# Kernel tuning notes

Hardware: AMD Instinct MI355X
Metric: run time of the kernel (lower is better)

## Reference

```python
import jax, jax.numpy as jnp
import numpy as np


def setup_inputs() -> dict:
    key = jax.random.key(0)
    k1, k2, k3, k4 = jax.random.split(key, 4)
    n, d, h, w = 16, 512, 64, 64
    m, kcodes = 4, 256
    dm = d // m  # 128
    latent = jax.random.normal(k1, (n, d, h, w), dtype=jnp.float32)
    codebook = jax.random.normal(k2, (m, kcodes, dm), dtype=jnp.float32)
    wq = jax.random.normal(k3, (m, dm, dm), dtype=jnp.float32) / np.sqrt(dm)
    wk = jax.random.normal(k4, (m, dm, dm), dtype=jnp.float32) / np.sqrt(dm)
    return {"latent": latent, "codebook": codebook, "wq": wq, "wk": wk}


def reference(latent, codebook, wq, wk):
    # latent: [n, d, h, w]; codebook: [m, k, dm]; wq/wk: [m, dm, dm]
    n, d, h, w = latent.shape
    m, kcodes, dm = codebook.shape
    # NCHW -> NHWC -> [n, h, w, m, dm]
    q = jnp.transpose(latent, (0, 2, 3, 1)).reshape(n, h, w, m, dm)
    # per-group query projection: q @ wq^T (einsum 'nhwmd,mcd->nhwmc')
    q = jnp.einsum('nhwmd,mcd->nhwmc', q, wq)
    # per-group key projection of codebook: 'mkd,mcd->mkc'
    keys = jnp.einsum('mkd,mcd->mkc', codebook, wk)
    # dot-product scores over code dim, then argmax -> code indices
    scores = jnp.einsum('nhwmd,mkd->nhwmk', q, keys)
    code = jnp.argmax(scores, axis=-1).astype(jnp.uint8)
    return code
```

## Files before the change

### kernel.cpp

```cpp
#include <hip/hip_runtime.h>


#define MM   4
#define KC   256
#define DM   128
#define HW   4096
#define WW_  64
#define EPS  0.045f
#define WL_CAP 65536
#define RSH  136

typedef _Float16 f16x8 __attribute__((ext_vector_type(8)));
typedef _Float16 f16x4 __attribute__((ext_vector_type(4)));
typedef _Float16 f16x2 __attribute__((ext_vector_type(2)));
typedef float    f32x4 __attribute__((ext_vector_type(4)));
typedef float    f32x2 __attribute__((ext_vector_type(2)));

__global__ __launch_bounds__(128) void a_kernel(const float* __restrict__ wk,
                                                const float* __restrict__ wq,
                                                double* __restrict__ A) {
    int me = blockIdx.x;
    int d  = threadIdx.x;
    int m  = me >> 7;
    int e  = me & 127;
    const float* wkm = wk + (size_t)m * DM * DM + e;
    const float* wqm = wq + (size_t)m * DM * DM + d;
    double s0 = 0.0, s1 = 0.0, s2 = 0.0, s3 = 0.0;
#pragma unroll 8
    for (int c = 0; c < DM; c += 4) {
        s0 = fma((double)wkm[(size_t)(c+0) * DM], (double)wqm[(size_t)(c+0) * DM], s0);
        s1 = fma((double)wkm[(size_t)(c+1) * DM], (double)wqm[(size_t)(c+1) * DM], s1);
        s2 = fma((double)wkm[(size_t)(c+2) * DM], (double)wqm[(size_t)(c+2) * DM], s2);
        s3 = fma((double)wkm[(size_t)(c+3) * DM], (double)wqm[(size_t)(c+3) * DM], s3);
    }
    A[(size_t)me * DM + d] = (s0 + s1) + (s2 + s3);
}

__global__ __launch_bounds__(128) void keff_kernel(const float* __restrict__ cb,
                                                   const double* __restrict__ A,
                                                   double* __restrict__ keffdT,
                                                   _Float16* __restrict__ keff16) {
    int mk = blockIdx.x;
    int d  = threadIdx.x;
    int m  = mk >> 8;
    int k  = mk & 255;
    const float*  cbr = cb + (size_t)mk * DM;
    const double* Am  = A + (size_t)m * DM * DM + d;
    double s0 = 0.0, s1 = 0.0, s2 = 0.0, s3 = 0.0;
#pragma unroll 8
    for (int e = 0; e < DM; e += 4) {
        s0 = fma((double)cbr[e+0], Am[(size_t)(e+0) * DM], s0);
        s1 = fma((double)cbr[e+1], Am[(size_t)(e+1) * DM], s1);
        s2 = fma((double)cbr[e+2], Am[(size_t)(e+2) * DM], s2);
        s3 = fma((double)cbr[e+3], Am[(size_t)(e+3) * DM], s3);
    }
    double s = (s0 + s1) + (s2 + s3);
    keffdT[((size_t)m * DM + d) * KC + k] = s;
    keff16[(size_t)mk * DM + d] = (_Float16)s;
}

__global__ __launch_bounds__(512, 4) void argmax_mfma(const float* __restrict__ latent,
                                                      const _Float16* __restrict__ keff16,
                                                      int* __restrict__ out,
                                                      int* __restrict__ wl_cnt,
                                                      int* __restrict__ wl) {
    __shared__ _Float16 lq[2][64 * RSH];
    __shared__ float pbv[64][8];
    __shared__ float psv[64][8];
    __shared__ int   pbi[64][8];

    int blk  = blockIdx.x;
    int n    = blk >> 5;
    int m    = (blk >> 3) & 3;
    int hg   = blk & 7;
    int tid  = threadIdx.x;
    int wave = tid >> 6;
    int lane = tid & 63;
    int col  = lane & 15;
    int quad = lane >> 4;
    int w2   = (tid & 31) * 2;
    int db   = (tid >> 5) * 8;

    f16x8 Af[2][4];
    {
        const _Float16* kbase = keff16 + ((size_t)m * KC + wave * 32) * DM;
#pragma unroll
        for (int t = 0; t < 2; ++t)
#pragma unroll
            for (int s = 0; s < 4; ++s)
                Af[t][s] = *(const f16x8*)(kbase + (size_t)(t * 16 + col) * DM + s * 32 + quad * 8);
    }

    const float* lp0 = latent + ((size_t)(n * 512 + m * DM)) * HW + (size_t)(hg * 8) * WW_;

    {
        f32x2 pf[8];
#pragma unroll
        for (int pp = 0; pp < 8; ++pp)
            pf[pp] = *(const f32x2*)(lp0 + (size_t)(db + pp) * HW + w2);
#pragma unroll
        for (int j = 0; j < 2; ++j) {
            f16x8 v;
#pragma unroll
            for (int pp = 0; pp < 8; ++pp) v[pp] = (_Float16)pf[pp][j];
            *(f16x8*)&lq[0][(size_t)(w2 + j) * RSH + db] = v;
        }
    }
    __syncthreads();

    for (int r = 0; r < 8; ++r) {
        int cur = r & 1;

        f32x2 pf[8];
        if (r < 7) {
            const float* lp = lp0 + (size_t)(r + 1) * WW_;
#pragma unroll
            for (int pp = 0; pp < 8; ++pp)
                pf[pp] = *(const f32x2*)(lp + (size_t)(db + pp) * HW + w2);
        }

#pragma unroll
        for (int p = 0; p < 4; ++p) {
            f16x8 Bf[4];
#pragma unroll
            for (int s = 0; s < 4; ++s)
                Bf[s] = *(const f16x8*)&lq[cur][(size_t)(p * 16 + col) * RSH + s * 32 + quad * 8];
            f32x4 acc[2];
#pragma unroll
            for (int t = 0; t < 2; ++t) {
                f32x4 c = (f32x4){0.f, 0.f, 0.f, 0.f};
                c = __builtin_amdgcn_mfma_f32_16x16x32_f16(Af[t][0], Bf[0], c, 0, 0, 0);
                c = __builtin_amdgcn_mfma_f32_16x16x32_f16(Af[t][1], Bf[1], c, 0, 0, 0);
                c = __builtin_amdgcn_mfma_f32_16x16x32_f16(Af[t][2], Bf[2], c, 0, 0, 0);
                c = __builtin_amdgcn_mfma_f32_16x16x32_f16(Af[t][3], Bf[3], c, 0, 0, 0);
                acc[t] = c;
            }
            float bv = acc[0][0];
            int   bi = wave * 32 + quad * 4;
            float sv = -3.0e38f;
#pragma unroll
            for (int t = 0; t < 2; ++t)
#pragma unroll
                for (int g = 0; g < 4; ++g) {
                    if (t == 0 && g == 0) continue;
                    float v   = acc[t][g];
                    int   idx = wave * 32 + t * 16 + quad * 4 + g;
                    if (v > bv)      { sv = bv; bv = v; bi = idx; }
                    else if (v > sv) sv = v;
                }
#pragma unroll
            for (int off = 16; off < 64; off <<= 1) {
                float ov = __shfl_xor(bv, off);
                int   oi = __shfl_xor(bi, off);
                float os = __shfl_xor(sv, off);
                bool  take  = (ov > bv) || (ov == bv && oi < bi);
                float loser = take ? bv : ov;
                sv = fmaxf(fmaxf(sv, os), loser);
                if (take) { bv = ov; bi = oi; }
            }
            if (quad == 0) {
                int P = p * 16 + col;
                pbv[P][wave] = bv; psv[P][wave] = sv; pbi[P][wave] = bi;
            }
        }
        __syncthreads();

        if (tid < 64) {
            int   P  = tid;
            float bv = pbv[P][0]; float sv = psv[P][0]; int bi = pbi[P][0];
#pragma unroll
            for (int wv = 1; wv < 8; ++wv) {
                float ov = pbv[P][wv]; float os = psv[P][wv]; int oi = pbi[P][wv];
                bool  take  = (ov > bv) || (ov == bv && oi < bi);
                float loser = take ? bv : ov;
                sv = fmaxf(fmaxf(sv, os), loser);
                if (take) { bv = ov; bi = oi; }
            }
            int h   = hg * 8 + r;
            int pix = (((n * 64 + h) * 64) + P) * MM + m;
            out[pix] = bi;
            if (bv - sv < EPS) {
                int slot = atomicAdd(wl_cnt, 1);
                if (slot < WL_CAP) wl[slot] = pix;
            }
        }

        if (r < 7) {
#pragma unroll
            for (int j = 0; j < 2; ++j) {
                f16x8 v;
#pragma unroll
                for (int pp = 0; pp < 8; ++pp) v[pp] = (_Float16)pf[pp][j];
                *(f16x8*)&lq[cur ^ 1][(size_t)(w2 + j) * RSH + db] = v;
            }
        }
        __syncthreads();
    }
}

__global__ __launch_bounds__(256) void rescue_kernel(const float* __restrict__ latent,
                                                     const double* __restrict__ keffdT,
                                                     const int* __restrict__ wl_cnt,
                                                     const int* __restrict__ wl,
                                                     int* __restrict__ out) {
    __shared__ double sq[DM];
    __shared__ double svals[256];
    __shared__ int    sidx[256];
    int cnt = *wl_cnt;
    if (cnt > WL_CAP) cnt = WL_CAP;
    int t = threadIdx.x;
    for (int i = blockIdx.x; i < cnt; i += gridDim.x) {
        int pix = wl[i];
        int m   = pix & 3;
        int rem = pix >> 2;
        int w   = rem & 63;
        int bh  = rem >> 6;
        int n   = bh >> 6;
        int h   = bh & 63;
        const float* lp = latent + ((size_t)(n * 512 + m * DM)) * HW + h * WW_ + w;
        if (t < DM) sq[t] = (double)lp[(size_t)t * HW];
        __syncthreads();
        const double* kr = keffdT + (size_t)m * DM * KC + t;
        double s0 = 0.0, s1 = 0.0, s2 = 0.0, s3 = 0.0;
#pragma unroll 8
        for (int d = 0; d < DM; d += 4) {
            s0 = fma(sq[d+0], kr[(size_t)(d+0) * KC], s0);
            s1 = fma(sq[d+1], kr[(size_t)(d+1) * KC], s1);
            s2 = fma(sq[d+2], kr[(size_t)(d+2) * KC], s2);
            s3 = fma(sq[d+3], kr[(size_t)(d+3) * KC], s3);
        }
        svals[t] = (s0 + s1) + (s2 + s3);
        sidx[t]  = t;
        __syncthreads();
        for (int stp = 128; stp > 0; stp >>= 1) {
            if (t < stp) {
                double vo = svals[t + stp], vm = svals[t];
                int io = sidx[t + stp], im = sidx[t];
                if (vo > vm || (vo == vm && io < im)) { svals[t] = vo; sidx[t] = io; }
            }
            __syncthreads();
        }
        if (t == 0) out[pix] = sidx[0];
        __syncthreads();
    }
}

extern "C" void kernel_launch(void* const* d_in, const int* in_sizes, int n_in,
                              void* d_out, int out_size, void* d_ws, size_t ws_size,
                              hipStream_t stream) {
    const float* latent = (const float*)d_in[0];
    const float* cb     = (const float*)d_in[1];
    const float* wq     = (const float*)d_in[2];
    const float* wk     = (const float*)d_in[3];
    int* out = (int*)d_out;

    char* ws = (char*)d_ws;
    double*   A      = (double*)ws;     ws += (size_t)MM * DM * DM * sizeof(double);
    double*   keffdT = (double*)ws;     ws += (size_t)MM * DM * KC * sizeof(double);
    _Float16* keff16 = (_Float16*)ws;   ws += (size_t)MM * KC * DM * sizeof(_Float16);
    int*      wl_cnt = (int*)ws;        ws += 256;
    int*      wl     = (int*)ws;

    hipMemsetAsync(wl_cnt, 0, sizeof(int), stream);
    a_kernel<<<MM * DM, 128, 0, stream>>>(wk, wq, A);
    keff_kernel<<<MM * KC, 128, 0, stream>>>(cb, A, keffdT, keff16);
    argmax_mfma<<<512, 512, 0, stream>>>(latent, keff16, out, wl_cnt, wl);
    rescue_kernel<<<1024, 256, 0, stream>>>(latent, keffdT, wl_cnt, wl, out);
}
```

Before: 276.3 us.

## Parallelize per-row argmax merge, split worklist per group, batch rescue pixels

In the MFMA argmax kernel the cross-wave merge now uses all 512 threads with shuffles instead of 64 threads looping. The partial buffers are double-buffered so one __syncthreads per row can be dropped, and the next-row LDS store is moved before the barrier. The rescue worklist is split per group m with separate padded counters to reduce atomic contention. Each rescue block now handles 4 pixels at once, so every keff row load is shared across them. Capacity per group drops to 16384 entries, which could overflow if near-tie pixels cluster in one group.

Result: faster. 253.6 us (-8.2%).

```diff
diff --git a/kernel.cpp b/kernel.cpp
--- a/kernel.cpp
+++ b/kernel.cpp
@@ -7,7 +7,8 @@
 #define HW   4096
 #define WW_  64
 #define EPS  0.045f
-#define WL_CAP 65536
+#define WLC  16384
+#define RPB  4
 #define RSH  136
 
 typedef _Float16 f16x8 __attribute__((ext_vector_type(8)));
@@ -65,9 +66,9 @@
                                                       int* __restrict__ wl_cnt,
                                                       int* __restrict__ wl) {
     __shared__ _Float16 lq[2][64 * RSH];
-    __shared__ float pbv[64][8];
-    __shared__ float psv[64][8];
-    __shared__ int   pbi[64][8];
+    __shared__ float pbv[2][64][8];
+    __shared__ float psv[2][64][8];
+    __shared__ int   pbi[2][64][8];
 
     int blk  = blockIdx.x;
     int n    = blk >> 5;
@@ -160,41 +161,47 @@
             }
             if (quad == 0) {
                 int P = p * 16 + col;
-                pbv[P][wave] = bv; psv[P][wave] = sv; pbi[P][wave] = bi;
-            }
-        }
-        __syncthreads();
-
-        if (tid < 64) {
-            int   P  = tid;
-            float bv = pbv[P][0]; float sv = psv[P][0]; int bi = pbi[P][0];
-#pragma unroll
-            for (int wv = 1; wv < 8; ++wv) {
-                float ov = pbv[P][wv]; float os = psv[P][wv]; int oi = pbi[P][wv];
+                pbv[cur][P][wave] = bv; psv[cur][P][wave] = sv; pbi[cur][P][wave] = bi;
+            }
+        }
+
+        if (r < 7) {
+#pragma unroll
+            for (int j = 0; j < 2; ++j) {
+                f16x8 v;
+#pragma unroll
+                for (int pp = 0; pp < 8; ++pp) v[pp] = (_Float16)pf[pp][j];
+                *(f16x8*)&lq[cur ^ 1][(size_t)(w2 + j) * RSH + db] = v;
+            }
+        }
+        __syncthreads();
+
+        {
+            int P    = tid >> 3;
+            int slot = tid & 7;
+            float bv = pbv[cur][P][slot];
+            float sv = psv[cur][P][slot];
+            int   bi = pbi[cur][P][slot];
+#pragma unroll
+            for (int off = 1; off < 8; off <<= 1) {
+                float ov = __shfl_xor(bv, off);
+                int   oi = __shfl_xor(bi, off);
+                float os = __shfl_xor(sv, off);
                 bool  take  = (ov > bv) || (ov == bv && oi < bi);
                 float loser = take ? bv : ov;
                 sv = fmaxf(fmaxf(sv, os), loser);
                 if (take) { bv = ov; bi = oi; }
             }
-            int h   = hg * 8 + r;
-            int pix = (((n * 64 + h) * 64) + P) * MM + m;
-            out[pix] = bi;
-            if (bv - sv < EPS) {
-                int slot = atomicAdd(wl_cnt, 1);
-                if (slot < WL_CAP) wl[slot] = pix;
-            }
-        }
-
-        if (r < 7) {
-#pragma unroll
-            for (int j = 0; j < 2; ++j) {
-                f16x8 v;
-#pragma unroll
-                for (int pp = 0; pp < 8; ++pp) v[pp] = (_Float16)pf[pp][j];
-                *(f16x8*)&lq[cur ^ 1][(size_t)(w2 + j) * RSH + db] = v;
-            }
-        }
-        __syncthreads();
+            if (slot == 0) {
+                int h   = hg * 8 + r;
+                int pix = (((n * 64 + h) * 64) + P) * MM + m;
+                out[pix] = bi;
+                if (bv - sv < EPS) {
+                    int s_ = atomicAdd(wl_cnt + m * 16, 1);
+                    if (s_ < WLC) wl[m * WLC + s_] = pix;
+                }
+            }
+        }
     }
 }
 
@@ -203,44 +210,63 @@
                                                      const int* __restrict__ wl_cnt,
                                                      const int* __restrict__ wl,
                                                      int* __restrict__ out) {
-    __shared__ double sq[DM];
-    __shared__ double svals[256];
-    __shared__ int    sidx[256];
-    int cnt = *wl_cnt;
-    if (cnt > WL_CAP) cnt = WL_CAP;
-    int t = threadIdx.x;
-    for (int i = blockIdx.x; i < cnt; i += gridDim.x) {
-        int pix = wl[i];
-        int m   = pix & 3;
+    __shared__ double sq[RPB][DM];
+    __shared__ double sval[256][RPB];
+    __shared__ int    sidx[256][RPB];
+    __shared__ int    spix[RPB];
+    int b   = blockIdx.x;
+    int m   = b & 3;
+    int t   = threadIdx.x;
+    int cnt = wl_cnt[m * 16];
+    if (cnt > WLC) cnt = WLC;
+    const int*    wlm = wl + m * WLC;
+    const double* krm = keffdT + (size_t)m * DM * KC + t;
+
+    for (int i0 = (b >> 2) * RPB; i0 < cnt; i0 += 256 * RPB) {
+        int pi  = t >> 6;
+        int dd  = (t & 63) * 2;
+        int idx = i0 + pi;
+        int vld = idx < cnt;
+        int pix = wlm[vld ? idx : i0];
         int rem = pix >> 2;
         int w   = rem & 63;
         int bh  = rem >> 6;
         int n   = bh >> 6;
         int h   = bh & 63;
         const float* lp = latent + ((size_t)(n * 512 + m * DM)) * HW + h * WW_ + w;
-        if (t < DM) sq[t] = (double)lp[(size_t)t * HW];
-        __syncthreads();
-        const double* kr = keffdT + (size_t)m * DM * KC + t;
+        sq[pi][dd]     = (double)lp[(size_t)dd * HW];
+        sq[pi][dd + 1] = (double)lp[(size_t)(dd + 1) * HW];
+        if ((t & 63) == 0) spix[pi] = vld ? pix : -1;
+        __syncthreads();
+
         double s0 = 0.0, s1 = 0.0, s2 = 0.0, s3 = 0.0;
-#pragma unroll 8
-        for (int d = 0; d < DM; d += 4) {
-            s0 = fma(sq[d+0], kr[(size_t)(d+0) * KC], s0);
-            s1 = fma(sq[d+1], kr[(size_t)(d+1) * KC], s1);
-            s2 = fma(sq[d+2], kr[(size_t)(d+2) * KC], s2);
-            s3 = fma(sq[d+3], kr[(size_t)(d+3) * KC], s3);
-        }
-        svals[t] = (s0 + s1) + (s2 + s3);
-        sidx[t]  = t;
-        __syncthreads();
+#pragma unroll 4
+        for (int d = 0; d < DM; ++d) {
+            double kd = krm[(size_t)d * KC];
+            s0 = fma(sq[0][d], kd, s0);
+            s1 = fma(sq[1][d], kd, s1);
+            s2 = fma(sq[2][d], kd, s2);
+            s3 = fma(sq[3][d], kd, s3);
+        }
+        sval[t][0] = s0; sval[t][1] = s1; sval[t][2] = s2; sval[t][3] = s3;
+        sidx[t][0] = t;  sidx[t][1] = t;  sidx[t][2] = t;  sidx[t][3] = t;
+        __syncthreads();
+
         for (int stp = 128; stp > 0; stp >>= 1) {
             if (t < stp) {
-                double vo = svals[t + stp], vm = svals[t];
-                int io = sidx[t + stp], im = sidx[t];
-                if (vo > vm || (vo == vm && io < im)) { svals[t] = vo; sidx[t] = io; }
+#pragma unroll
+                for (int p = 0; p < RPB; ++p) {
+                    double vo = sval[t + stp][p], vm = sval[t][p];
+                    int io = sidx[t + stp][p], im = sidx[t][p];
+                    if (vo > vm || (vo == vm && io < im)) { sval[t][p] = vo; sidx[t][p] = io; }
+                }
             }
             __syncthreads();
         }
-        if (t == 0) out[pix] = sidx[0];
+        if (t < RPB) {
+            int opix = spix[t];
+            if (opix >= 0) out[opix] = sidx[0][t];
+        }
         __syncthreads();
     }
 }
@@ -261,7 +287,7 @@
     int*      wl_cnt = (int*)ws;        ws += 256;
     int*      wl     = (int*)ws;
 
-    hipMemsetAsync(wl_cnt, 0, sizeof(int), stream);
+    hipMemsetAsync(wl_cnt, 0, 256, stream);
     a_kernel<<<MM * DM, 128, 0, stream>>>(wk, wq, A);
     keff_kernel<<<MM * KC, 128, 0, stream>>>(cb, A, keffdT, keff16);
     argmax_mfma<<<512, 512, 0, stream>>>(latent, keff16, out, wl_cnt, wl);
```
